# Optimization experiments

Hardware: AMD Instinct MI355X
Metric: run time of the kernel (lower is better)

## Reference

```python
import jax, jax.numpy as jnp
import numpy as np


def setup_inputs() -> dict:
    key = jax.random.key(0)
    k1, k2, k3, k4, k5 = jax.random.split(key, 5)
    b, l, h, dh, g, n = 2, 2048, 8, 64, 1, 64
    x = jax.random.normal(k1, (b, l, h, dh), dtype=jnp.float32)
    dt = jax.random.uniform(k2, (b, l, h), dtype=jnp.float32)
    # A must be negative (Mamba convention) so exp(segsum(A*dt)) is bounded
    A = -jnp.abs(jax.random.normal(k3, (h,), dtype=jnp.float32))
    B = jax.random.normal(k4, (b, l, g, n), dtype=jnp.float32)
    C = jax.random.normal(k5, (b, l, g, n), dtype=jnp.float32)
    return {"x": x, "dt": dt, "A": A, "B": B, "C": C, "chunk_size": 64}


def _forward(x, dt, A, B, C):
    b, l, h, dh = x.shape
    g = B.shape[2]
    rep = h // g
    # expand_groups_to_heads: repeat each group across its heads
    q = jnp.repeat(C, rep, axis=2).astype(jnp.float32)  # (b,l,h,n)
    k = jnp.repeat(B, rep, axis=2).astype(jnp.float32)  # (b,l,h,n)
    v = x.astype(jnp.float32)                            # (b,l,h,dh)
    adt = A * dt                                         # (b,l,h)

    # rotary on last dim; angles = cumsum(dt) broadcast over n//2 (NeoX half-split)
    half = q.shape[-1] // 2
    ang = jnp.cumsum(dt, axis=1)[..., None]              # (b,l,h,1)
    cos, sin = jnp.cos(ang), jnp.sin(ang)

    def rope(t):
        t1, t2 = t[..., :half], t[..., half:]
        return jnp.concatenate([t1 * cos - t2 * sin, t1 * sin + t2 * cos], axis=-1)

    q, k = rope(q), rope(k)

    # segsum decay: decay[b,h,l,s] = exp(sum_{s<t<=l} adt_t) for s<=l else 0
    a = adt.transpose(0, 2, 1)                           # (b,h,l)
    cs = jnp.cumsum(a, axis=-1)
    seg = cs[..., :, None] - cs[..., None, :]            # (b,h,l,l)
    causal = jnp.tril(jnp.ones((l, l), dtype=bool))
    decay = jnp.where(causal, jnp.exp(seg), 0.0)

    # trapezoidal scale with trap=0 (baseline passes zeros): w_s = 0.5*(1+exp(adt_s))
    w = 0.5 * (1.0 + jnp.exp(a))                         # (b,h,l)
    decay = decay * w[..., None, :]                      # scale each key position s

    scores = jnp.einsum('blhd,bshd->bhls', q, k) * decay
    y = jnp.einsum('bhls,bshd->blhd', scores, v)
    return y


def reference(x, dt, A, B, C, chunk_size):
    # chunk_size is unused by the quadratic (non-chunked) reference formulation
    return _forward(x, dt, A, B, C)
```

## Files before the change

### kernel.cpp

```cpp
#include <hip/hip_runtime.h>
#include <math.h>

constexpr int L_ = 2048;
constexpr int H_ = 8;
constexpr int BH_ = 16;
constexpr int TSZ = 64;
constexpr int NT_ = L_ / TSZ;
constexpr int CHUNK = 8;
constexpr int NCHP = NT_ / CHUNK;
constexpr float SKIP_THR = -15.f;

typedef __bf16 bf16x8 __attribute__((ext_vector_type(8)));
typedef __bf16 bf16x4 __attribute__((ext_vector_type(4)));
typedef float f32x4 __attribute__((ext_vector_type(4)));

constexpr size_t ANG_OFF = 0;
constexpr size_t SN_OFF  = ANG_OFF + (size_t)BH_ * L_;
constexpr size_t CS_OFF  = SN_OFF  + (size_t)BH_ * L_;
constexpr size_t SNW_OFF = CS_OFF  + (size_t)BH_ * L_;
constexpr size_t CSW_OFF = SNW_OFF + (size_t)BH_ * L_;
constexpr size_t PART_OFF = CSW_OFF + (size_t)BH_ * L_;

__device__ __forceinline__ int swz(int row, int d) {
    return row * 64 + ((((d >> 3) ^ (row & 7))) << 3) + (d & 7);
}

__global__ void scan_kernel(const float* __restrict__ dt, const float* __restrict__ A,
                            float* __restrict__ ws) {
    int bh = blockIdx.x;
    int b = bh >> 3, h = bh & 7;
    int t = threadIdx.x;
    __shared__ float part[256];
    const float* dtp = dt + (size_t)b * L_ * H_ + h;
    float v[8];
    float s = 0.f;
    int l0 = t * 8;
#pragma unroll
    for (int i = 0; i < 8; ++i) { v[i] = dtp[(size_t)(l0 + i) * H_]; s += v[i]; }
    part[t] = s;
    __syncthreads();
#pragma unroll
    for (int off = 1; off < 256; off <<= 1) {
        float add = (t >= off) ? part[t - off] : 0.f;
        __syncthreads();
        part[t] += add;
        __syncthreads();
    }
    float run = (t == 0) ? 0.f : part[t - 1];
    float Ah = A[h];
    size_t base = (size_t)bh * L_ + l0;
#pragma unroll
    for (int i = 0; i < 8; ++i) {
        run += v[i];
        float sn, cs;
        sincosf(run, &sn, &cs);
        float w = 0.5f * (1.f + __expf(Ah * v[i]));
        ws[ANG_OFF + base + i] = run;
        ws[SN_OFF  + base + i] = sn;
        ws[CS_OFF  + base + i] = cs;
        ws[SNW_OFF + base + i] = sn * w;
        ws[CSW_OFF + base + i] = cs * w;
    }
}

__launch_bounds__(256)
__global__ void attn_kernel(const float* __restrict__ x, const float* __restrict__ A,
                            const float* __restrict__ Bm, const float* __restrict__ Cm,
                            float* __restrict__ ws) {
    int rt = blockIdx.x, bh = blockIdx.y, cz = blockIdx.z;
    int cz_d = rt / CHUNK;
    if (cz > cz_d) return;
    bool diag = (cz == cz_d);
    int st_lo = cz * CHUNK;
    int b = bh >> 3, h = bh & 7;
    float Ah = A[h];
    int l0 = rt * TSZ;
    const float* angB = ws + ANG_OFF + (size_t)bh * L_;
    const float* snA  = ws + SN_OFF  + (size_t)bh * L_;
    const float* csA  = ws + CS_OFF  + (size_t)bh * L_;
    const float* snwA = ws + SNW_OFF + (size_t)bh * L_;
    const float* cswA = ws + CSW_OFF + (size_t)bh * L_;
    float angL0 = angB[l0];

    auto pred = [&](int st) {
        return Ah * (angL0 - angB[(size_t)st * TSZ + TSZ - 1]) >= SKIP_THR;
    };
    int st_hi = diag ? rt - 1 : st_lo + CHUNK - 1;
    if (!diag && !pred(st_hi)) return;

    __shared__ __align__(16) __bf16 lds_q[64 * 64];
    __shared__ __align__(16) __bf16 lds_k[64 * 64];
    __shared__ __align__(16) __bf16 lds_vt[64 * 72];
    __shared__ __align__(16) __bf16 lds_p[64 * 64];
    __shared__ float angRow[TSZ];
    __shared__ float colfac[TSZ];

    int t = threadIdx.x;
    int w = t >> 6, lane = t & 63, lg = lane >> 4, l15 = lane & 15;

    const float4* B4 = (const float4*)(Bm + (size_t)b * L_ * 64);
    const float4* C4 = (const float4*)(Cm + (size_t)b * L_ * 64);

#pragma unroll
    for (int it = 0; it < 2; ++it) {
        int wi = it * 256 + t;
        int r = wi >> 3, dq = wi & 7;
        int l = l0 + r;
        float4 lo = C4[(size_t)l * 16 + dq];
        float4 hi = C4[(size_t)l * 16 + dq + 8];
        float sn = snA[l], cs = csA[l];
        bf16x4 qlo = {(__bf16)(lo.x * cs - hi.x * sn), (__bf16)(lo.y * cs - hi.y * sn),
                      (__bf16)(lo.z * cs - hi.z * sn), (__bf16)(lo.w * cs - hi.w * sn)};
        bf16x4 qhi = {(__bf16)(lo.x * sn + hi.x * cs), (__bf16)(lo.y * sn + hi.y * cs),
                      (__bf16)(lo.z * sn + hi.z * cs), (__bf16)(lo.w * sn + hi.w * cs)};
        *(bf16x4*)&lds_q[swz(r, dq * 4)] = qlo;
        *(bf16x4*)&lds_q[swz(r, dq * 4 + 32)] = qhi;
    }
    if (t < TSZ) angRow[t] = angB[l0 + t];

    float4 pBlo[2], pBhi[2], pV[4];
    float pSnw[2], pCsw[2], pAng = 0.f;
    int sq = t >> 4, dqx = t & 15;

    auto prefetch = [&](int s0) {
#pragma unroll
        for (int it = 0; it < 2; ++it) {
            int wi = it * 256 + t;
            int r = wi >> 3, dq = wi & 7;
            int l = s0 + r;
            pBlo[it] = B4[(size_t)l * 16 + dq];
            pBhi[it] = B4[(size_t)l * 16 + dq + 8];
            pSnw[it] = snwA[l];
            pCsw[it] = cswA[l];
        }
        const float4* xv4 = (const float4*)(x + (((size_t)b * L_ + s0) * H_ + h) * 64);
#pragma unroll
        for (int i = 0; i < 4; ++i)
            pV[i] = xv4[(size_t)(sq * 4 + i) * 128 + dqx];
        if (t < TSZ) pAng = angB[s0 + t];
    };

    auto commit = [&]() {
#pragma unroll
        for (int it = 0; it < 2; ++it) {
            int wi = it * 256 + t;
            int r = wi >> 3, dq = wi & 7;
            float sw = pSnw[it], cw = pCsw[it];
            float4 lo = pBlo[it], hi = pBhi[it];
            bf16x4 klo = {(__bf16)(lo.x * cw - hi.x * sw), (__bf16)(lo.y * cw - hi.y * sw),
                          (__bf16)(lo.z * cw - hi.z * sw), (__bf16)(lo.w * cw - hi.w * sw)};
            bf16x4 khi = {(__bf16)(lo.x * sw + hi.x * cw), (__bf16)(lo.y * sw + hi.y * cw),
                          (__bf16)(lo.z * sw + hi.z * cw), (__bf16)(lo.w * sw + hi.w * cw)};
            *(bf16x4*)&lds_k[swz(r, dq * 4)] = klo;
            *(bf16x4*)&lds_k[swz(r, dq * 4 + 32)] = khi;
        }
#pragma unroll
        for (int j = 0; j < 4; ++j) {
            int d = dqx * 4 + j;
            bf16x4 vv = {(__bf16)((const float*)&pV[0])[j], (__bf16)((const float*)&pV[1])[j],
                         (__bf16)((const float*)&pV[2])[j], (__bf16)((const float*)&pV[3])[j]};
            *(bf16x4*)&lds_vt[d * 72 + sq * 4] = vv;
        }
        if (t < TSZ) colfac[t] = __expf(fminf(Ah * (angL0 - pAng), 0.f));
    };

    f32x4 accD[4] = {{0.f, 0.f, 0.f, 0.f}, {0.f, 0.f, 0.f, 0.f},
                     {0.f, 0.f, 0.f, 0.f}, {0.f, 0.f, 0.f, 0.f}};
    f32x4 accO[4] = {{0.f, 0.f, 0.f, 0.f}, {0.f, 0.f, 0.f, 0.f},
                     {0.f, 0.f, 0.f, 0.f}, {0.f, 0.f, 0.f, 0.f}};

    int qrow = w * 16 + l15;
    int rbase = w * 16 + lg * 4;

    auto s_mfma = [&](f32x4 (&sa)[4]) {
        bf16x8 a0 = *(const bf16x8*)&lds_q[swz(qrow, lg * 8)];
        bf16x8 a1 = *(const bf16x8*)&lds_q[swz(qrow, lg * 8 + 32)];
#pragma unroll
        for (int ng = 0; ng < 4; ++ng) {
            int srow = ng * 16 + l15;
            bf16x8 b0 = *(const bf16x8*)&lds_k[swz(srow, lg * 8)];
            bf16x8 b1 = *(const bf16x8*)&lds_k[swz(srow, lg * 8 + 32)];
            f32x4 z = {0.f, 0.f, 0.f, 0.f};
            z = __builtin_amdgcn_mfma_f32_16x16x32_bf16(a0, b0, z, 0, 0, 0);
            z = __builtin_amdgcn_mfma_f32_16x16x32_bf16(a1, b1, z, 0, 0, 0);
            sa[ng] = z;
        }
    };

    auto p_write = [&](f32x4 (&sa)[4]) {
#pragma unroll
        for (int ng = 0; ng < 4; ++ng)
#pragma unroll
            for (int reg = 0; reg < 4; ++reg)
                lds_p[swz(rbase + reg, ng * 16 + l15)] = (__bf16)sa[ng][reg];
    };

    auto pv_mfma = [&](f32x4 (&acc)[4]) {
        bf16x8 pa0 = *(const bf16x8*)&lds_p[swz(qrow, lg * 8)];
        bf16x8 pa1 = *(const bf16x8*)&lds_p[swz(qrow, lg * 8 + 32)];
#pragma unroll
        for (int ng = 0; ng < 4; ++ng) {
            int dl = ng * 16 + l15;
            bf16x8 v0 = *(const bf16x8*)&lds_vt[dl * 72 + lg * 8];
            bf16x8 v1 = *(const bf16x8*)&lds_vt[dl * 72 + lg * 8 + 32];
            acc[ng] = __builtin_amdgcn_mfma_f32_16x16x32_bf16(pa0, v0, acc[ng], 0, 0, 0);
            acc[ng] = __builtin_amdgcn_mfma_f32_16x16x32_bf16(pa1, v1, acc[ng], 0, 0, 0);
        }
    };

    int st;
    bool have_next;
    if (diag) {
        prefetch(l0);
        commit();
        st = rt - 1;
        have_next = (st >= st_lo) && pred(st);
        if (have_next) prefetch(st * TSZ);
        __syncthreads();
        f32x4 sa[4];
        s_mfma(sa);
        float ar[4];
#pragma unroll
        for (int reg = 0; reg < 4; ++reg) ar[reg] = angRow[rbase + reg];
#pragma unroll
        for (int ng = 0; ng < 4; ++ng) {
            int sl = ng * 16 + l15;
            float as = angRow[sl];
#pragma unroll
            for (int reg = 0; reg < 4; ++reg) {
                float dec = (sl <= rbase + reg) ? __expf(Ah * (ar[reg] - as)) : 0.f;
                sa[ng][reg] *= dec;
            }
        }
        p_write(sa);
        __syncthreads();
        pv_mfma(accD);
    } else {
        st = st_hi;
        have_next = true;
        prefetch(st * TSZ);
    }

    while (have_next) {
        __syncthreads();
        commit();
        int nst = st - 1;
        bool hn = (nst >= st_lo) && pred(nst);
        if (hn) prefetch(nst * TSZ);
        __syncthreads();
        f32x4 sa[4];
        s_mfma(sa);
#pragma unroll
        for (int ng = 0; ng < 4; ++ng) {
            float cf = colfac[ng * 16 + l15];
#pragma unroll
            for (int reg = 0; reg < 4; ++reg) sa[ng][reg] *= cf;
        }
        p_write(sa);
        __syncthreads();
        pv_mfma(accO);
        st = nst;
        have_next = hn;
    }

    float* pp = ws + PART_OFF + ((((size_t)rt * BH_ + bh) * NCHP + cz) << 12);
#pragma unroll
    for (int reg = 0; reg < 4; ++reg) {
        int rloc = rbase + reg;
        float rf = __expf(Ah * (angRow[rloc] - angL0));
#pragma unroll
        for (int ng = 0; ng < 4; ++ng)
            pp[(size_t)rloc * 64 + ng * 16 + l15] = accD[ng][reg] + rf * accO[ng][reg];
    }
}

__launch_bounds__(256)
__global__ void reduce_kernel(const float* __restrict__ ws, const float* __restrict__ A,
                              float* __restrict__ out) {
    int rt = blockIdx.x, bh = blockIdx.y;
    int b = bh >> 3, h = bh & 7;
    float Ah = A[h];
    const float* angB = ws + ANG_OFF + (size_t)bh * L_;
    int l0 = rt * TSZ;
    float angL0 = angB[l0];
    int cz_d = rt / CHUNK;
    int t = threadIdx.x;
    int r0 = (t >> 4) * 4, c0 = (t & 15) * 4;
    float acc[4][4] = {{0.f}};
    for (int cz = 0; cz <= cz_d; ++cz) {
        if (cz < cz_d) {
            int st_hi = cz * CHUNK + CHUNK - 1;
            if (!(Ah * (angL0 - angB[(size_t)st_hi * TSZ + TSZ - 1]) >= SKIP_THR))
                continue;
        }
        const float* pp = ws + PART_OFF + ((((size_t)rt * BH_ + bh) * NCHP + cz) << 12);
#pragma unroll
        for (int i = 0; i < 4; ++i) {
            float4 v = *(const float4*)&pp[(size_t)(r0 + i) * 64 + c0];
            acc[i][0] += v.x; acc[i][1] += v.y; acc[i][2] += v.z; acc[i][3] += v.w;
        }
    }
    float* op = out + (((size_t)b * L_ + l0) * H_ + h) * 64;
#pragma unroll
    for (int i = 0; i < 4; ++i)
        *(float4*)&op[(size_t)(r0 + i) * H_ * 64 + c0] =
            make_float4(acc[i][0], acc[i][1], acc[i][2], acc[i][3]);
}

extern "C" void kernel_launch(void* const* d_in, const int* in_sizes, int n_in,
                              void* d_out, int out_size, void* d_ws, size_t ws_size,
                              hipStream_t stream) {
    const float* x  = (const float*)d_in[0];
    const float* dt = (const float*)d_in[1];
    const float* A  = (const float*)d_in[2];
    const float* Bm = (const float*)d_in[3];
    const float* Cm = (const float*)d_in[4];
    float* ws = (float*)d_ws;
    float* out = (float*)d_out;

    scan_kernel<<<BH_, 256, 0, stream>>>(dt, A, ws);
    attn_kernel<<<dim3(NT_, BH_, NCHP), 256, 0, stream>>>(x, A, Bm, Cm, ws);
    reduce_kernel<<<dim3(NT_, BH_), 256, 0, stream>>>(ws, A, out);
}
```

Measured before the change: 103.0 us.

## Keep Q fragments in registers, drop redundant barriers, write solo tiles directly to output

Q is now loaded straight from global memory and rotated into MFMA A-operand registers, so the Q shared-memory tile and its per-iteration LDS reads go away. The barrier between writing P and the PV MFMA is removed, because each wave only reads back the P rows it wrote itself. Row tiles whose only non-skipped work is the diagonal chunk now write their result straight to the output, and the reduce kernel returns early for those tiles, saving a workspace round trip. CHUNK is halved to split the off-diagonal work across more blocks, at the cost of more partial buffers to sum for the remaining tiles.

After: 109.8 us. 1.07x slower.

```diff
diff --git a/kernel.cpp b/kernel.cpp
--- a/kernel.cpp
+++ b/kernel.cpp
@@ -6,7 +6,7 @@
 constexpr int BH_ = 16;
 constexpr int TSZ = 64;
 constexpr int NT_ = L_ / TSZ;
-constexpr int CHUNK = 8;
+constexpr int CHUNK = 4;
 constexpr int NCHP = NT_ / CHUNK;
 constexpr float SKIP_THR = -15.f;
 
@@ -66,7 +66,7 @@
 __launch_bounds__(256)
 __global__ void attn_kernel(const float* __restrict__ x, const float* __restrict__ A,
                             const float* __restrict__ Bm, const float* __restrict__ Cm,
-                            float* __restrict__ ws) {
+                            float* __restrict__ ws, float* __restrict__ out) {
     int rt = blockIdx.x, bh = blockIdx.y, cz = blockIdx.z;
     int cz_d = rt / CHUNK;
     if (cz > cz_d) return;
@@ -87,8 +87,8 @@
     };
     int st_hi = diag ? rt - 1 : st_lo + CHUNK - 1;
     if (!diag && !pred(st_hi)) return;
-
-    __shared__ __align__(16) __bf16 lds_q[64 * 64];
+    bool solo = diag && ((cz_d == 0) || !pred(cz_d * CHUNK - 1));
+
     __shared__ __align__(16) __bf16 lds_k[64 * 64];
     __shared__ __align__(16) __bf16 lds_vt[64 * 72];
     __shared__ __align__(16) __bf16 lds_p[64 * 64];
@@ -101,20 +101,26 @@
     const float4* B4 = (const float4*)(Bm + (size_t)b * L_ * 64);
     const float4* C4 = (const float4*)(Cm + (size_t)b * L_ * 64);
 
-#pragma unroll
-    for (int it = 0; it < 2; ++it) {
-        int wi = it * 256 + t;
-        int r = wi >> 3, dq = wi & 7;
-        int l = l0 + r;
-        float4 lo = C4[(size_t)l * 16 + dq];
-        float4 hi = C4[(size_t)l * 16 + dq + 8];
-        float sn = snA[l], cs = csA[l];
-        bf16x4 qlo = {(__bf16)(lo.x * cs - hi.x * sn), (__bf16)(lo.y * cs - hi.y * sn),
-                      (__bf16)(lo.z * cs - hi.z * sn), (__bf16)(lo.w * cs - hi.w * sn)};
-        bf16x4 qhi = {(__bf16)(lo.x * sn + hi.x * cs), (__bf16)(lo.y * sn + hi.y * cs),
-                      (__bf16)(lo.z * sn + hi.z * cs), (__bf16)(lo.w * sn + hi.w * cs)};
-        *(bf16x4*)&lds_q[swz(r, dq * 4)] = qlo;
-        *(bf16x4*)&lds_q[swz(r, dq * 4 + 32)] = qhi;
+    int qrow = w * 16 + l15;
+    int rbase = w * 16 + lg * 4;
+
+    bf16x8 qa0, qa1;
+    {
+        int ql = l0 + qrow;
+        float4 lo0 = C4[(size_t)ql * 16 + lg * 2];
+        float4 lo1 = C4[(size_t)ql * 16 + lg * 2 + 1];
+        float4 hi0 = C4[(size_t)ql * 16 + lg * 2 + 8];
+        float4 hi1 = C4[(size_t)ql * 16 + lg * 2 + 9];
+        float sn = snA[ql], cs = csA[ql];
+        const float* lo = (const float*)&lo0;
+        float lof[8] = {lo0.x, lo0.y, lo0.z, lo0.w, lo1.x, lo1.y, lo1.z, lo1.w};
+        float hif[8] = {hi0.x, hi0.y, hi0.z, hi0.w, hi1.x, hi1.y, hi1.z, hi1.w};
+        (void)lo;
+#pragma unroll
+        for (int j = 0; j < 8; ++j) {
+            qa0[j] = (__bf16)(lof[j] * cs - hif[j] * sn);
+            qa1[j] = (__bf16)(lof[j] * sn + hif[j] * cs);
+        }
     }
     if (t < TSZ) angRow[t] = angB[l0 + t];
 
@@ -169,20 +175,15 @@
     f32x4 accO[4] = {{0.f, 0.f, 0.f, 0.f}, {0.f, 0.f, 0.f, 0.f},
                      {0.f, 0.f, 0.f, 0.f}, {0.f, 0.f, 0.f, 0.f}};
 
-    int qrow = w * 16 + l15;
-    int rbase = w * 16 + lg * 4;
-
     auto s_mfma = [&](f32x4 (&sa)[4]) {
-        bf16x8 a0 = *(const bf16x8*)&lds_q[swz(qrow, lg * 8)];
-        bf16x8 a1 = *(const bf16x8*)&lds_q[swz(qrow, lg * 8 + 32)];
 #pragma unroll
         for (int ng = 0; ng < 4; ++ng) {
             int srow = ng * 16 + l15;
             bf16x8 b0 = *(const bf16x8*)&lds_k[swz(srow, lg * 8)];
             bf16x8 b1 = *(const bf16x8*)&lds_k[swz(srow, lg * 8 + 32)];
             f32x4 z = {0.f, 0.f, 0.f, 0.f};
-            z = __builtin_amdgcn_mfma_f32_16x16x32_bf16(a0, b0, z, 0, 0, 0);
-            z = __builtin_amdgcn_mfma_f32_16x16x32_bf16(a1, b1, z, 0, 0, 0);
+            z = __builtin_amdgcn_mfma_f32_16x16x32_bf16(qa0, b0, z, 0, 0, 0);
+            z = __builtin_amdgcn_mfma_f32_16x16x32_bf16(qa1, b1, z, 0, 0, 0);
             sa[ng] = z;
         }
     };
@@ -233,7 +234,6 @@
             }
         }
         p_write(sa);
-        __syncthreads();
         pv_mfma(accD);
     } else {
         st = st_hi;
@@ -257,20 +257,32 @@
             for (int reg = 0; reg < 4; ++reg) sa[ng][reg] *= cf;
         }
         p_write(sa);
-        __syncthreads();
         pv_mfma(accO);
         st = nst;
         have_next = hn;
     }
 
-    float* pp = ws + PART_OFF + ((((size_t)rt * BH_ + bh) * NCHP + cz) << 12);
-#pragma unroll
-    for (int reg = 0; reg < 4; ++reg) {
-        int rloc = rbase + reg;
-        float rf = __expf(Ah * (angRow[rloc] - angL0));
-#pragma unroll
-        for (int ng = 0; ng < 4; ++ng)
-            pp[(size_t)rloc * 64 + ng * 16 + l15] = accD[ng][reg] + rf * accO[ng][reg];
+    if (solo) {
+        float* op = out + (((size_t)b * L_ + l0) * H_ + h) * 64;
+#pragma unroll
+        for (int reg = 0; reg < 4; ++reg) {
+            int rloc = rbase + reg;
+            float rf = __expf(Ah * (angRow[rloc] - angL0));
+#pragma unroll
+            for (int ng = 0; ng < 4; ++ng)
+                op[(size_t)rloc * H_ * 64 + ng * 16 + l15] =
+                    accD[ng][reg] + rf * accO[ng][reg];
+        }
+    } else {
+        float* pp = ws + PART_OFF + ((((size_t)rt * BH_ + bh) * NCHP + cz) << 12);
+#pragma unroll
+        for (int reg = 0; reg < 4; ++reg) {
+            int rloc = rbase + reg;
+            float rf = __expf(Ah * (angRow[rloc] - angL0));
+#pragma unroll
+            for (int ng = 0; ng < 4; ++ng)
+                pp[(size_t)rloc * 64 + ng * 16 + l15] = accD[ng][reg] + rf * accO[ng][reg];
+        }
     }
 }
 
@@ -284,14 +296,18 @@
     int l0 = rt * TSZ;
     float angL0 = angB[l0];
     int cz_d = rt / CHUNK;
+    auto pred = [&](int st) {
+        return Ah * (angL0 - angB[(size_t)st * TSZ + TSZ - 1]) >= SKIP_THR;
+    };
+    if ((cz_d == 0) || !pred(cz_d * CHUNK - 1)) return;
+
     int t = threadIdx.x;
     int r0 = (t >> 4) * 4, c0 = (t & 15) * 4;
     float acc[4][4] = {{0.f}};
     for (int cz = 0; cz <= cz_d; ++cz) {
         if (cz < cz_d) {
             int st_hi = cz * CHUNK + CHUNK - 1;
-            if (!(Ah * (angL0 - angB[(size_t)st_hi * TSZ + TSZ - 1]) >= SKIP_THR))
-                continue;
+            if (!pred(st_hi)) continue;
         }
         const float* pp = ws + PART_OFF + ((((size_t)rt * BH_ + bh) * NCHP + cz) << 12);
 #pragma unroll
@@ -319,6 +335,6 @@
     float* out = (float*)d_out;
 
     scan_kernel<<<BH_, 256, 0, stream>>>(dt, A, ws);
-    attn_kernel<<<dim3(NT_, BH_, NCHP), 256, 0, stream>>>(x, A, Bm, Cm, ws);
+    attn_kernel<<<dim3(NT_, BH_, NCHP), 256, 0, stream>>>(x, A, Bm, Cm, ws, out);
     reduce_kernel<<<dim3(NT_, BH_), 256, 0, stream>>>(ws, A, out);
 }
```
